# Kernel tuning notes

Measured on AMD Instinct MI355X. Metric: run time of the kernel, lower is better.

The kernel has to match this reference:

```python
import jax, jax.numpy as jnp
import numpy as np

DIM = 1024
BATCH = 8
SEQ = 4096


def setup_inputs() -> dict:
    key = jax.random.key(0)
    ks = jax.random.split(key, 9)
    s = 0.1  # torch init used randn*0.1 for A,B; linears use small init too
    return {
        "x": jax.random.normal(ks[0], (BATCH, SEQ, DIM), jnp.float32),
        "A": jax.random.normal(ks[1], (DIM, DIM), jnp.float32) * s,
        "B": jax.random.normal(ks[2], (DIM, DIM), jnp.float32) * s,
        "W_in": jax.random.normal(ks[3], (DIM, DIM), jnp.float32) * (1.0 / np.sqrt(DIM)),
        "b_in": jax.random.normal(ks[4], (DIM,), jnp.float32) * 0.01,
        "W_gate": jax.random.normal(ks[5], (DIM, DIM), jnp.float32) * (1.0 / np.sqrt(DIM)),
        "b_gate": jax.random.normal(ks[6], (DIM,), jnp.float32) * 0.01,
        "W_out": jax.random.normal(ks[7], (DIM, DIM), jnp.float32) * (1.0 / np.sqrt(DIM)),
        "b_out": jax.random.normal(ks[8], (DIM,), jnp.float32) * 0.01,
    }


def reference(x, A, B, W_in, b_in, W_gate, b_gate, W_out, b_out):
    # x: (batch, seq, dim). Precompute time-parallel parts outside the scan.
    inp = jnp.einsum("bsd,ed->bse", x, W_in) + b_in            # in_proj(x_t)
    gate = jax.nn.sigmoid(jnp.einsum("bsd,ed->bse", inp, W_gate) + b_gate)
    u = jnp.einsum("bsd,ed->bse", inp, B)                      # inp @ B.T, hoisted

    # scan over time for the nonlinear recurrence
    def step(state, tg):
        inp_t, gate_t, u_t = tg                                # each (batch, dim)
        blended = gate_t * state + (1.0 - gate_t) * inp_t
        new_state = jnp.tanh(blended @ A.T + u_t)              # dropout p=0 -> identity
        return new_state, new_state

    state0 = jnp.zeros((x.shape[0], x.shape[2]), x.dtype)
    xs = (inp.transpose(1, 0, 2), gate.transpose(1, 0, 2), u.transpose(1, 0, 2))
    _, states = jax.lax.scan(step, state0, xs)                 # (seq, batch, dim)

    out = jnp.einsum("sbd,ed->sbe", states, W_out) + b_out     # out_proj, hoisted
    return out.transpose(1, 0, 2)                              # (batch, seq, dim)
```

## Files before the change

### kernel.cpp

```cpp
#include <hip/hip_runtime.h>
#include <stdint.h>
#include <stddef.h>


#define DIM   1024
#define SEQ   4096
#define NB    8
#define NTOK  (NB*SEQ)

typedef __attribute__((ext_vector_type(8))) short          short8;
typedef __attribute__((ext_vector_type(4))) float          float4v;
typedef __attribute__((ext_vector_type(4))) int            int4v;
typedef __attribute__((ext_vector_type(4))) unsigned short ushort4v;

__device__ __forceinline__ unsigned short f2b(float f) {
  union { float f; unsigned int u; } v; v.f = f;
  return (unsigned short)((v.u + 0x7FFFu + ((v.u >> 16) & 1u)) >> 16);
}
__device__ __forceinline__ float b2f(unsigned short h) {
  union { unsigned int u; float f; } v; v.u = ((unsigned int)h) << 16;
  return v.f;
}

__global__ void cast_bf16(const float* __restrict__ src,
                          unsigned short* __restrict__ dst, int n) {
  int i4 = (blockIdx.x * blockDim.x + threadIdx.x) * 4;
  if (i4 >= n) return;
  float4v v = *(const float4v*)(src + i4);
  ushort4v o;
  o[0] = f2b(v[0]); o[1] = f2b(v[1]); o[2] = f2b(v[2]); o[3] = f2b(v[3]);
  *(ushort4v*)(dst + i4) = o;
}

__global__ void build_wcat(const float* __restrict__ Bm, const float* __restrict__ A,
                           unsigned short* __restrict__ Wcat,
                           unsigned short* __restrict__ Ab) {
  int i4 = (blockIdx.x * 256 + threadIdx.x) * 4;
  int e = i4 >> 10, d = i4 & 1023;
  float4v bv = *(const float4v*)(Bm + i4);
  float4v av = *(const float4v*)(A + i4);
  ushort4v bb, ab;
  #pragma unroll
  for (int r = 0; r < 4; r++) { bb[r] = f2b(bv[r]); ab[r] = f2b(av[r]); }
  *(ushort4v*)(Wcat + (size_t)e * 2048 + d) = bb;
  *(ushort4v*)(Wcat + (size_t)e * 2048 + 1024 + d) = ab;
  *(ushort4v*)(Ab + i4) = ab;
}

__global__ void zero_u32(unsigned int* __restrict__ p, int n) {
  int i = blockIdx.x * 256 + threadIdx.x;
  if (i < n) p[i] = 0u;
}

template<int EPI>
__global__ __launch_bounds__(256, 2)
void gemm_nt(const unsigned short* __restrict__ Ag, int lda,
             const unsigned short* __restrict__ Bg, int ldb,
             int K,
             const float* __restrict__ bias,
             void* __restrict__ out0,
             unsigned short* __restrict__ out1,
             const unsigned short* __restrict__ aux) {
  __shared__ unsigned short sA[128 * 72];
  __shared__ unsigned short sB[128 * 72];
  const int tid  = threadIdx.x;
  const int lane = tid & 63;
  const int wave = tid >> 6;
  const int wm = wave & 1, wn = wave >> 1;
  const int m0 = blockIdx.x * 128;
  const int n0 = blockIdx.y * 128;
  const int q  = lane >> 4;
  const int ln = lane & 15;

  float4v acc[4][4];
  const float4v fz = {0.f, 0.f, 0.f, 0.f};
  #pragma unroll
  for (int i = 0; i < 4; i++)
    #pragma unroll
    for (int j = 0; j < 4; j++) acc[i][j] = fz;

  for (int kk = 0; kk < K; kk += 64) {
    __syncthreads();
    #pragma unroll
    for (int s = 0; s < 4; s++) {
      int chunk = tid + s * 256;
      int row = chunk >> 3, c = chunk & 7;
      int4v va = *(const int4v*)(Ag + (size_t)(m0 + row) * lda + kk + c * 8);
      int4v vb = *(const int4v*)(Bg + (size_t)(n0 + row) * ldb + kk + c * 8);
      *(int4v*)(sA + row * 72 + c * 8) = va;
      *(int4v*)(sB + row * 72 + c * 8) = vb;
    }
    __syncthreads();
    #pragma unroll
    for (int ks = 0; ks < 64; ks += 32) {
      short8 af[4], bf[4];
      #pragma unroll
      for (int i = 0; i < 4; i++)
        af[i] = *(const short8*)(sA + (wm * 64 + i * 16 + ln) * 72 + ks + q * 8);
      #pragma unroll
      for (int j = 0; j < 4; j++)
        bf[j] = *(const short8*)(sB + (wn * 64 + j * 16 + ln) * 72 + ks + q * 8);
      #pragma unroll
      for (int i = 0; i < 4; i++)
        #pragma unroll
        for (int j = 0; j < 4; j++)
          acc[i][j] = __builtin_amdgcn_mfma_f32_16x16x32_bf16(af[i], bf[j], acc[i][j], 0, 0, 0);
    }
  }

  #pragma unroll
  for (int j = 0; j < 4; j++) {
    const int gn = n0 + wn * 64 + j * 16 + ln;
    const float bval = (EPI == 2) ? 0.f : bias[gn];
    #pragma unroll
    for (int i = 0; i < 4; i++) {
      const int gm = m0 + wm * 64 + i * 16 + q * 4;
      #pragma unroll
      for (int r = 0; r < 4; r++) {
        const int row = gm + r;
        float vv = acc[i][j][r] + bval;
        if constexpr (EPI == 0) {
          ((unsigned short*)out0)[(size_t)row * 2048 + gn] = f2b(vv);
        } else if constexpr (EPI == 1) {
          float g = 1.f / (1.f + __expf(-vv));
          int t = row & (SEQ - 1), b = row >> 12;
          ((unsigned short*)out0)[(size_t)(t * NB + b) * DIM + gn] = f2b(g);
          float iv = b2f(aux[(size_t)row * 2048 + gn]);
          out1[(size_t)row * 2048 + 1024 + gn] = f2b((1.f - g) * iv);
        } else if constexpr (EPI == 2) {
          int t = row & (SEQ - 1), b = row >> 12;
          ((float*)out0)[(size_t)(t * NB + b) * DIM + gn] = vv;
        } else {
          int b = row & 7, t = row >> 3;
          ((float*)out0)[(size_t)(b * SEQ + t) * DIM + gn] = vv;
        }
      }
    }
  }
}

__global__ __launch_bounds__(256, 1)
void scan_kernel(const unsigned short* __restrict__ Ab,
                 const unsigned short* __restrict__ gscan,
                 const float* __restrict__ vflat,
                 unsigned short* __restrict__ sb,
                 unsigned short* __restrict__ mbuf,
                 unsigned int* __restrict__ flags) {
  const int tid  = threadIdx.x;
  const int lane = tid & 63;
  const int wave = tid >> 6;
  const int gw   = blockIdx.x * 4 + wave;
  const int e0   = gw * 16;
  const int q    = lane >> 4;
  const int ln   = lane & 15;
  const int bcl  = ln & 7;
  const bool active = (ln < 8);
  const int eb = e0 + q * 4;

  short8 af[32];
  #pragma unroll
  for (int ks = 0; ks < 32; ks++)
    af[ks] = *(const short8*)(Ab + (size_t)(e0 + ln) * 1024 + ks * 32 + q * 8);

  const unsigned int* fpoll = flags + lane;
  unsigned int* const myflag = flags + gw;
  const float4v fz = {0.f, 0.f, 0.f, 0.f};

  for (int t = 0; t < SEQ; t++) {
    float4v vv = fz;
    ushort4v g4 = {0, 0, 0, 0};
    size_t rowoff = (size_t)(t * NB + bcl) * DIM + eb;
    if (active) {
      vv = *(const float4v*)(vflat + rowoff);
      if (t < SEQ - 1)
        g4 = *(const ushort4v*)(gscan + (size_t)((t + 1) * NB + bcl) * DIM + eb);
    }

    {
      const unsigned int target = (unsigned int)t;
      for (;;) {
        unsigned int pv;
        asm volatile("global_load_dword %0, %1, off sc0 sc1\n\t"
                     "s_waitcnt vmcnt(0)"
                     : "=v"(pv) : "v"(fpoll) : "memory");
        if (__all((int)(pv >= target))) break;
      }
    }

    const unsigned short* mb = mbuf + (size_t)(t & 1) * (NB * DIM);
    const unsigned short* mbp = mb + bcl * DIM + q * 8;
    short8 fr[32];
    #pragma unroll
    for (int ks = 0; ks < 32; ks++)
      asm volatile("global_load_dwordx4 %0, %1, off offset:%2 sc0 sc1"
                   : "=v"(fr[ks]) : "v"(mbp), "n"(ks * 64));

    float4v a0 = fz, a1 = fz, a2 = fz, a3 = fz;
    #pragma unroll
    for (int c = 0; c < 8; c++) {
      asm volatile("s_waitcnt vmcnt(%4)"
                   : "+v"(fr[4 * c]), "+v"(fr[4 * c + 1]),
                     "+v"(fr[4 * c + 2]), "+v"(fr[4 * c + 3])
                   : "n"(28 - 4 * c));
      a0 = __builtin_amdgcn_mfma_f32_16x16x32_bf16(af[4 * c + 0], fr[4 * c + 0], a0, 0, 0, 0);
      a1 = __builtin_amdgcn_mfma_f32_16x16x32_bf16(af[4 * c + 1], fr[4 * c + 1], a1, 0, 0, 0);
      a2 = __builtin_amdgcn_mfma_f32_16x16x32_bf16(af[4 * c + 2], fr[4 * c + 2], a2, 0, 0, 0);
      a3 = __builtin_amdgcn_mfma_f32_16x16x32_bf16(af[4 * c + 3], fr[4 * c + 3], a3, 0, 0, 0);
    }

    if (active) {
      float sv[4];
      #pragma unroll
      for (int r = 0; r < 4; r++) {
        float xx = a0[r] + a1[r] + a2[r] + a3[r] + vv[r];
        float ex = __expf(-2.f * fabsf(xx));
        float th = (1.f - ex) / (1.f + ex);
        sv[r] = copysignf(th, xx);
      }
      ushort4v sp;
      #pragma unroll
      for (int r = 0; r < 4; r++) sp[r] = f2b(sv[r]);
      *(ushort4v*)(sb + rowoff) = sp;
      if (t < SEQ - 1) {
        unsigned long long mv =
            (unsigned long long)((unsigned int)f2b(b2f(g4[0]) * sv[0]) |
                                 ((unsigned int)f2b(b2f(g4[1]) * sv[1]) << 16)) |
            ((unsigned long long)((unsigned int)f2b(b2f(g4[2]) * sv[2]) |
                                  ((unsigned int)f2b(b2f(g4[3]) * sv[3]) << 16)) << 32);
        unsigned short* mn = mbuf + (size_t)((t + 1) & 1) * (NB * DIM) + bcl * DIM + eb;
        asm volatile("global_store_dwordx2 %0, %1, off sc0 sc1"
                     :: "v"(mn), "v"(mv) : "memory");
      }
    }

    if (t == SEQ - 1) break;

    asm volatile("s_waitcnt vmcnt(0)" ::: "memory");
    if (lane == 0) {
      unsigned int fv = (unsigned int)(t + 1);
      asm volatile("global_store_dword %0, %1, off sc0 sc1"
                   :: "v"(myflag), "v"(fv) : "memory");
    }
  }
}

extern "C" void kernel_launch(void* const* d_in, const int* in_sizes, int n_in,
                              void* d_out, int out_size, void* d_ws, size_t ws_size,
                              hipStream_t stream) {
  const float* x      = (const float*)d_in[0];
  const float* A      = (const float*)d_in[1];
  const float* Bm     = (const float*)d_in[2];
  const float* W_in   = (const float*)d_in[3];
  const float* b_in   = (const float*)d_in[4];
  const float* W_gate = (const float*)d_in[5];
  const float* b_gate = (const float*)d_in[6];
  const float* W_out  = (const float*)d_in[7];
  const float* b_out  = (const float*)d_in[8];

  char* ws = (char*)d_ws;
  unsigned short* xb      = (unsigned short*)(ws);
  unsigned short* inpq    = (unsigned short*)(ws + 67108864);
  unsigned short* gscan   = (unsigned short*)(ws + 201326592);
  unsigned short* Wb_in   = (unsigned short*)(ws + 268435456);
  unsigned short* Wb_gate = (unsigned short*)(ws + 270532608);
  unsigned short* Wb_out  = (unsigned short*)(ws + 272629760);
  unsigned short* Wcat    = (unsigned short*)(ws + 274726912);
  unsigned short* Ab      = (unsigned short*)(ws + 278921216);
  unsigned short* mbuf    = (unsigned short*)(ws + 281018368);
  unsigned int*   flags   = (unsigned int*)(ws + 281051136);
  float*          vflat   = (float*)d_out;
  unsigned short* sbuf    = xb;

  cast_bf16<<<(33554432 / 4 + 255) / 256, 256, 0, stream>>>(x, xb, 33554432);
  cast_bf16<<<1024, 256, 0, stream>>>(W_in,   Wb_in,   1048576);
  cast_bf16<<<1024, 256, 0, stream>>>(W_gate, Wb_gate, 1048576);
  cast_bf16<<<1024, 256, 0, stream>>>(W_out,  Wb_out,  1048576);
  build_wcat<<<1024, 256, 0, stream>>>(Bm, A, Wcat, Ab);
  zero_u32<<<(8192 + 64 + 255) / 256, 256, 0, stream>>>((unsigned int*)mbuf, 8192 + 64);

  dim3 grid(NTOK / 128, DIM / 128);
  gemm_nt<0><<<grid, 256, 0, stream>>>(xb, DIM, Wb_in, DIM, DIM, b_in,
                                       (void*)inpq, nullptr, nullptr);
  gemm_nt<1><<<grid, 256, 0, stream>>>(inpq, 2048, Wb_gate, DIM, DIM, b_gate,
                                       (void*)gscan, inpq, inpq);
  gemm_nt<2><<<grid, 256, 0, stream>>>(inpq, 2048, Wcat, 2048, 2048, b_in,
                                       (void*)vflat, nullptr, nullptr);
  scan_kernel<<<16, 256, 0, stream>>>(Ab, gscan, vflat, sbuf, mbuf, flags);
  gemm_nt<3><<<grid, 256, 0, stream>>>(sbuf, DIM, Wb_out, DIM, DIM, b_out,
                                       (void*)d_out, nullptr, nullptr);
}
```

Baseline: 29.39 ms.

## Co-locate scan workgroups on one XCD and sync through shared L2 only

The scan kernel now launches 256 workgroups, reads the XCD id from a hardware register, and keeps the first 16 workgroups that land on the first XCD to fill up. All others exit. Those 16 run a coherence self-test and, if it passes, use a fast path whose flag polls and state exchanges use only sc0 (XCD L2 scope) instead of system-coherent sc0 sc1. This is meant to cut the latency of each of the 4096 cross-workgroup synchronisation steps. A poison word and an iteration timeout fall back to the original system-coherent path, which brings extra complexity, dual stores on the slow path, and a reliance on undocumented workgroup placement and cache behaviour.

```diff
diff --git a/kernel.cpp b/kernel.cpp
--- a/kernel.cpp
+++ b/kernel.cpp
@@ -47,9 +47,9 @@
   *(ushort4v*)(Ab + i4) = ab;
 }
 
-__global__ void zero_u32(unsigned int* __restrict__ p, int n) {
+__global__ void init_ws(unsigned int* __restrict__ p, int n, int widx) {
   int i = blockIdx.x * 256 + threadIdx.x;
-  if (i < n) p[i] = 0u;
+  if (i < n) p[i] = (i == widx) ? 0xFFFFFFFFu : 0u;
 }
 
 template<int EPI>
@@ -139,21 +139,17 @@
   }
 }
 
-__global__ __launch_bounds__(256, 1)
-void scan_kernel(const unsigned short* __restrict__ Ab,
-                 const unsigned short* __restrict__ gscan,
-                 const float* __restrict__ vflat,
-                 unsigned short* __restrict__ sb,
-                 unsigned short* __restrict__ mbuf,
-                 unsigned int* __restrict__ flags) {
-  const int tid  = threadIdx.x;
-  const int lane = tid & 63;
-  const int wave = tid >> 6;
-  const int gw   = blockIdx.x * 4 + wave;
-  const int e0   = gw * 16;
-  const int q    = lane >> 4;
-  const int ln   = lane & 15;
-  const int bcl  = ln & 7;
+__device__ void scan_llc(const int t0, const int gw, const int lane,
+                         const unsigned short* __restrict__ Ab,
+                         const unsigned short* __restrict__ gscan,
+                         const float* __restrict__ vflat,
+                         unsigned short* __restrict__ sb,
+                         unsigned short* __restrict__ mbuf,
+                         unsigned int* __restrict__ flags) {
+  const int e0  = gw * 16;
+  const int q   = lane >> 4;
+  const int ln  = lane & 15;
+  const int bcl = ln & 7;
   const bool active = (ln < 8);
   const int eb = e0 + q * 4;
 
@@ -166,7 +162,7 @@
   unsigned int* const myflag = flags + gw;
   const float4v fz = {0.f, 0.f, 0.f, 0.f};
 
-  for (int t = 0; t < SEQ; t++) {
+  for (int t = t0; t < SEQ; t++) {
     float4v vv = fz;
     ushort4v g4 = {0, 0, 0, 0};
     size_t rowoff = (size_t)(t * NB + bcl) * DIM + eb;
@@ -228,6 +224,8 @@
             ((unsigned long long)((unsigned int)f2b(b2f(g4[2]) * sv[2]) |
                                   ((unsigned int)f2b(b2f(g4[3]) * sv[3]) << 16)) << 32);
         unsigned short* mn = mbuf + (size_t)((t + 1) & 1) * (NB * DIM) + bcl * DIM + eb;
+        asm volatile("global_store_dwordx2 %0, %1, off sc0"
+                     :: "v"(mn), "v"(mv) : "memory");
         asm volatile("global_store_dwordx2 %0, %1, off sc0 sc1"
                      :: "v"(mn), "v"(mv) : "memory");
       }
@@ -238,9 +236,237 @@
     asm volatile("s_waitcnt vmcnt(0)" ::: "memory");
     if (lane == 0) {
       unsigned int fv = (unsigned int)(t + 1);
+      asm volatile("global_store_dword %0, %1, off sc0"
+                   :: "v"(myflag), "v"(fv) : "memory");
       asm volatile("global_store_dword %0, %1, off sc0 sc1"
                    :: "v"(myflag), "v"(fv) : "memory");
     }
+  }
+}
+
+__device__ int scan_fast(const int gw, const int lane,
+                         const unsigned short* __restrict__ Ab,
+                         const unsigned short* __restrict__ gscan,
+                         const float* __restrict__ vflat,
+                         unsigned short* __restrict__ sb,
+                         unsigned short* __restrict__ mbuf,
+                         unsigned int* __restrict__ flags,
+                         unsigned int* __restrict__ poisonw) {
+  const int e0  = gw * 16;
+  const int q   = lane >> 4;
+  const int ln  = lane & 15;
+  const int bcl = ln & 7;
+  const bool active = (ln < 8);
+  const int eb = e0 + q * 4;
+
+  short8 af[32];
+  #pragma unroll
+  for (int ks = 0; ks < 32; ks++)
+    af[ks] = *(const short8*)(Ab + (size_t)(e0 + ln) * 1024 + ks * 32 + q * 8);
+
+  const unsigned int* fpoll = flags + lane;
+  unsigned int* const myflag = flags + gw;
+  const float4v fz = {0.f, 0.f, 0.f, 0.f};
+
+  for (int t = 0; t < SEQ; t++) {
+    float4v vv = fz;
+    ushort4v g4 = {0, 0, 0, 0};
+    size_t rowoff = (size_t)(t * NB + bcl) * DIM + eb;
+    if (active) {
+      vv = *(const float4v*)(vflat + rowoff);
+      if (t < SEQ - 1)
+        g4 = *(const ushort4v*)(gscan + (size_t)((t + 1) * NB + bcl) * DIM + eb);
+    }
+
+    const unsigned int target = (unsigned int)t;
+    bool bail = false;
+    {
+      unsigned int iters = 0;
+      for (;;) {
+        unsigned int pv, po;
+        asm volatile("global_load_dword %0, %2, off sc0\n\t"
+                     "global_load_dword %1, %3, off sc0\n\t"
+                     "s_waitcnt vmcnt(0)"
+                     : "=&v"(pv), "=&v"(po)
+                     : "v"(fpoll), "v"(poisonw) : "memory");
+        if (__all((int)(pv >= target))) break;
+        if (po != 0u) { bail = true; break; }
+        if (++iters >= 8192u) {
+          if (lane == 0) {
+            unsigned int one = 1u;
+            asm volatile("global_store_dword %0, %1, off sc0"
+                         :: "v"(poisonw), "v"(one) : "memory");
+            asm volatile("global_store_dword %0, %1, off sc0 sc1"
+                         :: "v"(poisonw), "v"(one) : "memory");
+          }
+          bail = true; break;
+        }
+      }
+    }
+    if (bail) {
+      if (active) {
+        #pragma unroll
+        for (int par = 0; par < 2; par++) {
+          unsigned short* mp = mbuf + (size_t)par * (NB * DIM) + bcl * DIM + eb;
+          unsigned long long mv_;
+          asm volatile("global_load_dwordx2 %0, %1, off sc0\n\t"
+                       "s_waitcnt vmcnt(0)"
+                       : "=&v"(mv_) : "v"(mp) : "memory");
+          asm volatile("global_store_dwordx2 %0, %1, off sc0 sc1"
+                       :: "v"(mp), "v"(mv_) : "memory");
+        }
+      }
+      asm volatile("s_waitcnt vmcnt(0)" ::: "memory");
+      if (lane == 0)
+        asm volatile("global_store_dword %0, %1, off sc0 sc1"
+                     :: "v"(myflag), "v"(target) : "memory");
+      return t;
+    }
+
+    const unsigned short* mb = mbuf + (size_t)(t & 1) * (NB * DIM);
+    const unsigned short* mbp = mb + bcl * DIM + q * 8;
+    short8 fr[32];
+    if (active) {
+      #pragma unroll
+      for (int ks = 0; ks < 32; ks++)
+        asm volatile("global_load_dwordx4 %0, %1, off offset:%2 sc0"
+                     : "=v"(fr[ks]) : "v"(mbp), "n"(ks * 64));
+    }
+
+    float4v a0 = fz, a1 = fz, a2 = fz, a3 = fz;
+    #pragma unroll
+    for (int c = 0; c < 8; c++) {
+      asm volatile("s_waitcnt vmcnt(%4)"
+                   : "+v"(fr[4 * c]), "+v"(fr[4 * c + 1]),
+                     "+v"(fr[4 * c + 2]), "+v"(fr[4 * c + 3])
+                   : "n"(28 - 4 * c));
+      a0 = __builtin_amdgcn_mfma_f32_16x16x32_bf16(af[4 * c + 0], fr[4 * c + 0], a0, 0, 0, 0);
+      a1 = __builtin_amdgcn_mfma_f32_16x16x32_bf16(af[4 * c + 1], fr[4 * c + 1], a1, 0, 0, 0);
+      a2 = __builtin_amdgcn_mfma_f32_16x16x32_bf16(af[4 * c + 2], fr[4 * c + 2], a2, 0, 0, 0);
+      a3 = __builtin_amdgcn_mfma_f32_16x16x32_bf16(af[4 * c + 3], fr[4 * c + 3], a3, 0, 0, 0);
+    }
+
+    if (active) {
+      float sv[4];
+      #pragma unroll
+      for (int r = 0; r < 4; r++) {
+        float xx = a0[r] + a1[r] + a2[r] + a3[r] + vv[r];
+        float ex = __expf(-2.f * fabsf(xx));
+        float th = (1.f - ex) / (1.f + ex);
+        sv[r] = copysignf(th, xx);
+      }
+      ushort4v sp;
+      #pragma unroll
+      for (int r = 0; r < 4; r++) sp[r] = f2b(sv[r]);
+      *(ushort4v*)(sb + rowoff) = sp;
+      if (t < SEQ - 1) {
+        unsigned long long mv =
+            (unsigned long long)((unsigned int)f2b(b2f(g4[0]) * sv[0]) |
+                                 ((unsigned int)f2b(b2f(g4[1]) * sv[1]) << 16)) |
+            ((unsigned long long)((unsigned int)f2b(b2f(g4[2]) * sv[2]) |
+                                  ((unsigned int)f2b(b2f(g4[3]) * sv[3]) << 16)) << 32);
+        unsigned short* mn = mbuf + (size_t)((t + 1) & 1) * (NB * DIM) + bcl * DIM + eb;
+        asm volatile("global_store_dwordx2 %0, %1, off sc0"
+                     :: "v"(mn), "v"(mv) : "memory");
+      }
+    }
+
+    if (t == SEQ - 1) break;
+
+    asm volatile("s_waitcnt vmcnt(0)" ::: "memory");
+    if (lane == 0) {
+      unsigned int fv = (unsigned int)(t + 1);
+      asm volatile("global_store_dword %0, %1, off sc0"
+                   :: "v"(myflag), "v"(fv) : "memory");
+    }
+  }
+  return SEQ;
+}
+
+__global__ __launch_bounds__(256, 1)
+void scan_kernel(const unsigned short* __restrict__ Ab,
+                 const unsigned short* __restrict__ gscan,
+                 const float* __restrict__ vflat,
+                 unsigned short* __restrict__ sb,
+                 unsigned short* __restrict__ mbuf,
+                 unsigned int* __restrict__ flags,
+                 unsigned int* __restrict__ ctl) {
+  const int tid  = threadIdx.x;
+  const int lane = tid & 63;
+  const int wave = tid >> 6;
+
+  __shared__ int s_rank, s_mode;
+  if (tid == 0) {
+    unsigned int xcd = __builtin_amdgcn_s_getreg(63508) & 15u;
+    int* winner = (int*)(ctl + 16);
+    unsigned int r = __hip_atomic_fetch_add(&ctl[xcd], 1u,
+                        __ATOMIC_RELAXED, __HIP_MEMORY_SCOPE_AGENT);
+    if (r == 15u) {
+      int expected = -1;
+      __hip_atomic_compare_exchange_strong(winner, &expected, (int)xcd,
+          __ATOMIC_RELAXED, __ATOMIC_RELAXED, __HIP_MEMORY_SCOPE_AGENT);
+    }
+    int w;
+    for (;;) {
+      w = __hip_atomic_load(winner, __ATOMIC_RELAXED, __HIP_MEMORY_SCOPE_AGENT);
+      if (w != -1) break;
+      __builtin_amdgcn_s_sleep(8);
+    }
+    int rank = (r < 16u && (int)xcd == w) ? (int)r : -1;
+
+    int mode = 1;
+    if (rank >= 0) {
+      unsigned int* sig    = ctl + 18;
+      unsigned int* ready1 = ctl + 17;
+      unsigned int* ready2 = ctl + 34;
+      unsigned int* ready3 = ctl + 35;
+      unsigned int* fail   = ctl + 36;
+      int ok = 1;
+      const unsigned int pats[2] = {0xC0DE0000u, 0xFEED0000u};
+      unsigned int* readys[2] = {ready1, ready2};
+      for (int ph = 0; ph < 2; ph++) {
+        unsigned int pat = pats[ph] | (unsigned int)rank;
+        const unsigned int* pw = sig + rank;
+        asm volatile("global_store_dword %0, %1, off sc0\n\t"
+                     "s_waitcnt vmcnt(0)"
+                     :: "v"(pw), "v"(pat) : "memory");
+        __hip_atomic_fetch_add(readys[ph], 1u,
+            __ATOMIC_SEQ_CST, __HIP_MEMORY_SCOPE_AGENT);
+        while (__hip_atomic_load(readys[ph],
+                 __ATOMIC_ACQUIRE, __HIP_MEMORY_SCOPE_AGENT) < 16u)
+          __builtin_amdgcn_s_sleep(2);
+        for (int i = 0; i < 16; i++) {
+          unsigned int v;
+          const unsigned int* pp = sig + i;
+          asm volatile("global_load_dword %0, %1, off sc0\n\t"
+                       "s_waitcnt vmcnt(0)"
+                       : "=&v"(v) : "v"(pp) : "memory");
+          if (v != (pats[ph] | (unsigned int)i)) ok = 0;
+        }
+      }
+      if (!ok)
+        __hip_atomic_fetch_add(fail, 1u, __ATOMIC_SEQ_CST, __HIP_MEMORY_SCOPE_AGENT);
+      __hip_atomic_fetch_add(ready3, 1u, __ATOMIC_SEQ_CST, __HIP_MEMORY_SCOPE_AGENT);
+      while (__hip_atomic_load(ready3,
+               __ATOMIC_ACQUIRE, __HIP_MEMORY_SCOPE_AGENT) < 16u)
+        __builtin_amdgcn_s_sleep(2);
+      mode = (__hip_atomic_load(fail,
+               __ATOMIC_ACQUIRE, __HIP_MEMORY_SCOPE_AGENT) != 0u) ? 1 : 0;
+    }
+    s_rank = rank;
+    s_mode = mode;
+  }
+  __syncthreads();
+  const int rank = s_rank;
+  if (rank < 0) return;
+  const int gw = rank * 4 + wave;
+
+  if (s_mode == 0) {
+    int tr = scan_fast(gw, lane, Ab, gscan, vflat, sb, mbuf, flags, ctl + 40);
+    if (tr < SEQ)
+      scan_llc(tr, gw, lane, Ab, gscan, vflat, sb, mbuf, flags);
+  } else {
+    scan_llc(0, gw, lane, Ab, gscan, vflat, sb, mbuf, flags);
   }
 }
 
@@ -268,6 +494,7 @@
   unsigned short* Ab      = (unsigned short*)(ws + 278921216);
   unsigned short* mbuf    = (unsigned short*)(ws + 281018368);
   unsigned int*   flags   = (unsigned int*)(ws + 281051136);
+  unsigned int*   ctl     = flags + 64;
   float*          vflat   = (float*)d_out;
   unsigned short* sbuf    = xb;
 
@@ -276,7 +503,7 @@
   cast_bf16<<<1024, 256, 0, stream>>>(W_gate, Wb_gate, 1048576);
   cast_bf16<<<1024, 256, 0, stream>>>(W_out,  Wb_out,  1048576);
   build_wcat<<<1024, 256, 0, stream>>>(Bm, A, Wcat, Ab);
-  zero_u32<<<(8192 + 64 + 255) / 256, 256, 0, stream>>>((unsigned int*)mbuf, 8192 + 64);
+  init_ws<<<(8320 + 255) / 256, 256, 0, stream>>>((unsigned int*)mbuf, 8320, 8272);
 
   dim3 grid(NTOK / 128, DIM / 128);
   gemm_nt<0><<<grid, 256, 0, stream>>>(xb, DIM, Wb_in, DIM, DIM, b_in,
@@ -285,7 +512,7 @@
                                        (void*)gscan, inpq, inpq);
   gemm_nt<2><<<grid, 256, 0, stream>>>(inpq, 2048, Wcat, 2048, 2048, b_in,
                                        (void*)vflat, nullptr, nullptr);
-  scan_kernel<<<16, 256, 0, stream>>>(Ab, gscan, vflat, sbuf, mbuf, flags);
+  scan_kernel<<<256, 256, 0, stream>>>(Ab, gscan, vflat, sbuf, mbuf, flags, ctl);
   gemm_nt<3><<<grid, 256, 0, stream>>>(sbuf, DIM, Wb_out, DIM, DIM, b_out,
                                        (void*)d_out, nullptr, nullptr);
 }
```

Result: slower. 40.75 ms (+38.6%).

## Replace flag barrier in scan with tag-embedded data polling

Applied to the files above, without the earlier changes.

The scan kernel no longer publishes a per-wave flag after draining its stores and then polls all flags before loading the shared state. Each 16-byte store now carries the step index as a tag next to the packed bf16 state values. Consumers load the state directly in eight pipelined groups and re-issue a group only when its tags do not yet match the current step, feeding MFMAs as each group becomes valid. This is meant to remove one global round trip and a full store drain from every sequential step. In exchange it doubles the bytes moved per step, depends on 16-byte stores being visible atomically, and gives up after a bounded number of retries.

```diff
diff --git a/kernel.cpp b/kernel.cpp
--- a/kernel.cpp
+++ b/kernel.cpp
@@ -139,13 +139,63 @@
   }
 }
 
+
+template<int G>
+__device__ __forceinline__ void issue8(const char* cb, int4v* s) {
+  #pragma unroll
+  for (int j = 0; j < 4; j++) {
+    asm volatile("global_load_dwordx4 %0, %1, off offset:%2 sc0 sc1"
+                 : "=v"(s[2 * j])     : "v"(cb), "n"(G * 512 + j * 128));
+    asm volatile("global_load_dwordx4 %0, %1, off offset:%2 sc0 sc1"
+                 : "=v"(s[2 * j + 1]) : "v"(cb), "n"(G * 512 + j * 128 + 16));
+  }
+}
+
+#define WAITV8(s)                                                   \
+  asm volatile("s_waitcnt vmcnt(8)"                                 \
+    : "+v"((s)[0]), "+v"((s)[1]), "+v"((s)[2]), "+v"((s)[3]),       \
+      "+v"((s)[4]), "+v"((s)[5]), "+v"((s)[6]), "+v"((s)[7]) :: "memory")
+#define WAITV0(s)                                                   \
+  asm volatile("s_waitcnt vmcnt(0)"                                 \
+    : "+v"((s)[0]), "+v"((s)[1]), "+v"((s)[2]), "+v"((s)[3]),       \
+      "+v"((s)[4]), "+v"((s)[5]), "+v"((s)[6]), "+v"((s)[7]) :: "memory")
+
+template<int G>
+__device__ __forceinline__ void consume_group(const char* cb, int4v* sl,
+                                              const short8* af, float4v* aa,
+                                              const int tgt) {
+  int4v* sg = sl + ((G & 1) * 8);
+  if constexpr (G < 7) issue8<G + 1>(cb, sl + (((G + 1) & 1) * 8));
+  if constexpr (G < 7) { WAITV8(sg); } else { WAITV0(sg); }
+  int tries = 0;
+  for (;;) {
+    int bad = 0;
+    #pragma unroll
+    for (int j = 0; j < 4; j++) {
+      bad |= (sg[2 * j][0] ^ tgt) | (sg[2 * j][3] ^ tgt) |
+             (sg[2 * j + 1][0] ^ tgt) | (sg[2 * j + 1][3] ^ tgt);
+    }
+    if (__all(bad == 0) || ++tries > 256) break;
+    __builtin_amdgcn_s_sleep(2);
+    issue8<G>(cb, sg);
+    WAITV0(sg);
+  }
+  #pragma unroll
+  for (int j = 0; j < 4; j++) {
+    int4v fd;
+    fd[0] = sg[2 * j][1];     fd[1] = sg[2 * j][2];
+    fd[2] = sg[2 * j + 1][1]; fd[3] = sg[2 * j + 1][2];
+    union { int4v i; short8 s; } cv; cv.i = fd;
+    aa[j] = __builtin_amdgcn_mfma_f32_16x16x32_bf16(af[4 * G + j], cv.s, aa[j], 0, 0, 0);
+  }
+}
+
 __global__ __launch_bounds__(256, 1)
 void scan_kernel(const unsigned short* __restrict__ Ab,
                  const unsigned short* __restrict__ gscan,
                  const float* __restrict__ vflat,
                  unsigned short* __restrict__ sb,
-                 unsigned short* __restrict__ mbuf,
-                 unsigned int* __restrict__ flags) {
+                 char* __restrict__ mtag) {
   const int tid  = threadIdx.x;
   const int lane = tid & 63;
   const int wave = tid >> 6;
@@ -162,8 +212,8 @@
   for (int ks = 0; ks < 32; ks++)
     af[ks] = *(const short8*)(Ab + (size_t)(e0 + ln) * 1024 + ks * 32 + q * 8);
 
-  const unsigned int* fpoll = flags + lane;
-  unsigned int* const myflag = flags + gw;
+  const int   cload = bcl * 4096 + q * 32;
+  const int   pslot = (bcl * 1024 + eb) * 4;
   const float4v fz = {0.f, 0.f, 0.f, 0.f};
 
   for (int t = 0; t < SEQ; t++) {
@@ -176,43 +226,24 @@
         g4 = *(const ushort4v*)(gscan + (size_t)((t + 1) * NB + bcl) * DIM + eb);
     }
 
-    {
-      const unsigned int target = (unsigned int)t;
-      for (;;) {
-        unsigned int pv;
-        asm volatile("global_load_dword %0, %1, off sc0 sc1\n\t"
-                     "s_waitcnt vmcnt(0)"
-                     : "=v"(pv) : "v"(fpoll) : "memory");
-        if (__all((int)(pv >= target))) break;
-      }
-    }
-
-    const unsigned short* mb = mbuf + (size_t)(t & 1) * (NB * DIM);
-    const unsigned short* mbp = mb + bcl * DIM + q * 8;
-    short8 fr[32];
-    #pragma unroll
-    for (int ks = 0; ks < 32; ks++)
-      asm volatile("global_load_dwordx4 %0, %1, off offset:%2 sc0 sc1"
-                   : "=v"(fr[ks]) : "v"(mbp), "n"(ks * 64));
-
-    float4v a0 = fz, a1 = fz, a2 = fz, a3 = fz;
-    #pragma unroll
-    for (int c = 0; c < 8; c++) {
-      asm volatile("s_waitcnt vmcnt(%4)"
-                   : "+v"(fr[4 * c]), "+v"(fr[4 * c + 1]),
-                     "+v"(fr[4 * c + 2]), "+v"(fr[4 * c + 3])
-                   : "n"(28 - 4 * c));
-      a0 = __builtin_amdgcn_mfma_f32_16x16x32_bf16(af[4 * c + 0], fr[4 * c + 0], a0, 0, 0, 0);
-      a1 = __builtin_amdgcn_mfma_f32_16x16x32_bf16(af[4 * c + 1], fr[4 * c + 1], a1, 0, 0, 0);
-      a2 = __builtin_amdgcn_mfma_f32_16x16x32_bf16(af[4 * c + 2], fr[4 * c + 2], a2, 0, 0, 0);
-      a3 = __builtin_amdgcn_mfma_f32_16x16x32_bf16(af[4 * c + 3], fr[4 * c + 3], a3, 0, 0, 0);
-    }
+    const char* cb = mtag + ((t & 1) << 15) + cload;
+    int4v sl[16];
+    issue8<0>(cb, sl);
+    float4v aa[4] = {fz, fz, fz, fz};
+    consume_group<0>(cb, sl, af, aa, t);
+    consume_group<1>(cb, sl, af, aa, t);
+    consume_group<2>(cb, sl, af, aa, t);
+    consume_group<3>(cb, sl, af, aa, t);
+    consume_group<4>(cb, sl, af, aa, t);
+    consume_group<5>(cb, sl, af, aa, t);
+    consume_group<6>(cb, sl, af, aa, t);
+    consume_group<7>(cb, sl, af, aa, t);
 
     if (active) {
       float sv[4];
       #pragma unroll
       for (int r = 0; r < 4; r++) {
-        float xx = a0[r] + a1[r] + a2[r] + a3[r] + vv[r];
+        float xx = aa[0][r] + aa[1][r] + aa[2][r] + aa[3][r] + vv[r];
         float ex = __expf(-2.f * fabsf(xx));
         float th = (1.f - ex) / (1.f + ex);
         sv[r] = copysignf(th, xx);
@@ -222,24 +253,16 @@
       for (int r = 0; r < 4; r++) sp[r] = f2b(sv[r]);
       *(ushort4v*)(sb + rowoff) = sp;
       if (t < SEQ - 1) {
-        unsigned long long mv =
-            (unsigned long long)((unsigned int)f2b(b2f(g4[0]) * sv[0]) |
-                                 ((unsigned int)f2b(b2f(g4[1]) * sv[1]) << 16)) |
-            ((unsigned long long)((unsigned int)f2b(b2f(g4[2]) * sv[2]) |
-                                  ((unsigned int)f2b(b2f(g4[3]) * sv[3]) << 16)) << 32);
-        unsigned short* mn = mbuf + (size_t)((t + 1) & 1) * (NB * DIM) + bcl * DIM + eb;
-        asm volatile("global_store_dwordx2 %0, %1, off sc0 sc1"
-                     :: "v"(mn), "v"(mv) : "memory");
+        int d0 = (int)((unsigned int)f2b(b2f(g4[0]) * sv[0]) |
+                       ((unsigned int)f2b(b2f(g4[1]) * sv[1]) << 16));
+        int d1 = (int)((unsigned int)f2b(b2f(g4[2]) * sv[2]) |
+                       ((unsigned int)f2b(b2f(g4[3]) * sv[3]) << 16));
+        int4v st;
+        st[0] = t + 1; st[1] = d0; st[2] = d1; st[3] = t + 1;
+        char* mp = mtag + (((t + 1) & 1) << 15) + pslot;
+        asm volatile("global_store_dwordx4 %0, %1, off sc0 sc1"
+                     :: "v"(mp), "v"(st) : "memory");
       }
-    }
-
-    if (t == SEQ - 1) break;
-
-    asm volatile("s_waitcnt vmcnt(0)" ::: "memory");
-    if (lane == 0) {
-      unsigned int fv = (unsigned int)(t + 1);
-      asm volatile("global_store_dword %0, %1, off sc0 sc1"
-                   :: "v"(myflag), "v"(fv) : "memory");
     }
   }
 }
@@ -266,8 +289,7 @@
   unsigned short* Wb_out  = (unsigned short*)(ws + 272629760);
   unsigned short* Wcat    = (unsigned short*)(ws + 274726912);
   unsigned short* Ab      = (unsigned short*)(ws + 278921216);
-  unsigned short* mbuf    = (unsigned short*)(ws + 281018368);
-  unsigned int*   flags   = (unsigned int*)(ws + 281051136);
+  char*           mtag    = (char*)inpq;
   float*          vflat   = (float*)d_out;
   unsigned short* sbuf    = xb;
 
@@ -276,7 +298,6 @@
   cast_bf16<<<1024, 256, 0, stream>>>(W_gate, Wb_gate, 1048576);
   cast_bf16<<<1024, 256, 0, stream>>>(W_out,  Wb_out,  1048576);
   build_wcat<<<1024, 256, 0, stream>>>(Bm, A, Wcat, Ab);
-  zero_u32<<<(8192 + 64 + 255) / 256, 256, 0, stream>>>((unsigned int*)mbuf, 8192 + 64);
 
   dim3 grid(NTOK / 128, DIM / 128);
   gemm_nt<0><<<grid, 256, 0, stream>>>(xb, DIM, Wb_in, DIM, DIM, b_in,
@@ -285,7 +306,8 @@
                                        (void*)gscan, inpq, inpq);
   gemm_nt<2><<<grid, 256, 0, stream>>>(inpq, 2048, Wcat, 2048, 2048, b_in,
                                        (void*)vflat, nullptr, nullptr);
-  scan_kernel<<<16, 256, 0, stream>>>(Ab, gscan, vflat, sbuf, mbuf, flags);
-  gemm_nt<3><<<grid, 256, 0, stream>>>(sbuf, DIM, Wb_out, DIM, DIM, b_out,
+  zero_u32<<<(16384 + 255) / 256, 256, 0, stream>>>((unsigned int*)mtag, 16384);
+  scan_kernel<<<16, 256, 0, stream>>>(Ab, gscan, vflat, sbuf, mtag);
+  gemm_nt<3><<<grid, 256, 0, stream>>>(sbuf, Wb_out == nullptr ? DIM : DIM, Wb_out, DIM, DIM, b_out,
                                        (void*)d_out, nullptr, nullptr);
 }
```

Result: slower. 39.30 ms (+33.7%).

## Use per-block flags with LDS fan-out and prefetch next-step inputs in scan

Applied to the files above, without the earlier changes.

The scan's cross-workgroup sync changes from one flag per wave polled by all 64 lanes to one flag per block. Only wave 0 polls the 16 block flags and then releases the other waves through a shared-memory variable, and a block barrier runs before the flag store. The per-step v and gate loads are issued one step ahead so they overlap the spin-wait and the MFMA chain instead of sitting on the critical path. This cuts global polling traffic on the serial recurrence, at the cost of an extra intra-block barrier and LDS spin per step.

```diff
diff --git a/kernel.cpp b/kernel.cpp
--- a/kernel.cpp
+++ b/kernel.cpp
@@ -157,35 +157,49 @@
   const bool active = (ln < 8);
   const int eb = e0 + q * 4;
 
+  __shared__ volatile int sready;
+  if (tid == 0) sready = 0;
+  __syncthreads();
+
   short8 af[32];
   #pragma unroll
   for (int ks = 0; ks < 32; ks++)
     af[ks] = *(const short8*)(Ab + (size_t)(e0 + ln) * 1024 + ks * 32 + q * 8);
 
-  const unsigned int* fpoll = flags + lane;
-  unsigned int* const myflag = flags + gw;
+  const unsigned int* fpoll = flags + (lane & 15);
+  unsigned int* const myflag = flags + blockIdx.x;
   const float4v fz = {0.f, 0.f, 0.f, 0.f};
 
+  float4v vv = fz;
+  ushort4v g4 = {0, 0, 0, 0};
+  if (active) {
+    vv = *(const float4v*)(vflat + (size_t)bcl * DIM + eb);
+    g4 = *(const ushort4v*)(gscan + (size_t)(NB + bcl) * DIM + eb);
+  }
+
   for (int t = 0; t < SEQ; t++) {
-    float4v vv = fz;
-    ushort4v g4 = {0, 0, 0, 0};
-    size_t rowoff = (size_t)(t * NB + bcl) * DIM + eb;
-    if (active) {
-      vv = *(const float4v*)(vflat + rowoff);
-      if (t < SEQ - 1)
-        g4 = *(const ushort4v*)(gscan + (size_t)((t + 1) * NB + bcl) * DIM + eb);
-    }
-
-    {
+    if (wave == 0) {
       const unsigned int target = (unsigned int)t;
       for (;;) {
         unsigned int pv;
         asm volatile("global_load_dword %0, %1, off sc0 sc1\n\t"
                      "s_waitcnt vmcnt(0)"
-                     : "=v"(pv) : "v"(fpoll) : "memory");
+                     : "=&v"(pv) : "v"(fpoll) : "memory");
         if (__all((int)(pv >= target))) break;
       }
-    }
+      sready = t;
+    } else {
+      while (sready < t) { }
+    }
+
+    const int tn = (t + 1 < SEQ) ? t + 1 : SEQ - 1;
+    const int tg = (t + 2 < SEQ) ? t + 2 : SEQ - 1;
+    const float* vp = vflat + (size_t)(tn * NB + bcl) * DIM + eb;
+    const unsigned short* gp = gscan + (size_t)(tg * NB + bcl) * DIM + eb;
+    float4v vv_n;
+    ushort4v g4_n;
+    asm volatile("global_load_dwordx4 %0, %1, off" : "=v"(vv_n) : "v"(vp));
+    asm volatile("global_load_dwordx2 %0, %1, off" : "=v"(g4_n) : "v"(gp));
 
     const unsigned short* mb = mbuf + (size_t)(t & 1) * (NB * DIM);
     const unsigned short* mbp = mb + bcl * DIM + q * 8;
@@ -209,6 +223,7 @@
     }
 
     if (active) {
+      size_t rowoff = (size_t)(t * NB + bcl) * DIM + eb;
       float sv[4];
       #pragma unroll
       for (int r = 0; r < 4; r++) {
@@ -233,10 +248,14 @@
       }
     }
 
+    vv = vv_n;
+    g4 = g4_n;
+
     if (t == SEQ - 1) break;
 
     asm volatile("s_waitcnt vmcnt(0)" ::: "memory");
-    if (lane == 0) {
+    __builtin_amdgcn_s_barrier();
+    if (tid == 0) {
       unsigned int fv = (unsigned int)(t + 1);
       asm volatile("global_store_dword %0, %1, off sc0 sc1"
                    :: "v"(myflag), "v"(fv) : "memory");
@@ -276,7 +295,7 @@
   cast_bf16<<<1024, 256, 0, stream>>>(W_gate, Wb_gate, 1048576);
   cast_bf16<<<1024, 256, 0, stream>>>(W_out,  Wb_out,  1048576);
   build_wcat<<<1024, 256, 0, stream>>>(Bm, A, Wcat, Ab);
-  zero_u32<<<(8192 + 64 + 255) / 256, 256, 0, stream>>>((unsigned int*)mbuf, 8192 + 64);
+  zero_u32<<<(8208 + 255) / 256, 256, 0, stream>>>((unsigned int*)mbuf, 8208);
 
   dim3 grid(NTOK / 128, DIM / 128);
   gemm_nt<0><<<grid, 256, 0, stream>>>(xb, DIM, Wb_in, DIM, DIM, b_in,
```

After: 25.66 ms. 1.15x faster.
